# Kernel optimization log

Measured on AMD Instinct MI355X. Metric: run time of the kernel, lower is better.

Reference implementation:

```python
import jax, jax.numpy as jnp
import numpy as np

B, S, E, H = 2, 2048, 1024, 16
DH = E // H  # 64


def setup_inputs() -> dict:
    key = jax.random.key(0)
    ks = jax.random.split(key, 9)
    scale = 1.0 / np.sqrt(E)
    q = jax.random.normal(ks[0], (B, S, E), jnp.float32)
    k = jax.random.normal(ks[1], (B, S, E), jnp.float32)
    v = jax.random.normal(ks[2], (B, S, E), jnp.float32)
    Wq = jax.random.uniform(ks[3], (E, E), jnp.float32, -scale, scale)
    Wk = jax.random.uniform(ks[4], (E, E), jnp.float32, -scale, scale)
    Wv = jax.random.uniform(ks[5], (E, E), jnp.float32, -scale, scale)
    bq = jax.random.uniform(ks[6], (E,), jnp.float32, -scale, scale)
    bk = jax.random.uniform(ks[7], (E,), jnp.float32, -scale, scale)
    bv = jax.random.uniform(ks[8], (E,), jnp.float32, -scale, scale)
    # causal mask: True = masked. [b, s_q, s_k]
    causal = jnp.triu(jnp.ones((S, S), bool), k=1)
    mask = jnp.broadcast_to(causal, (B, S, S))
    return {"q": q, "k": k, "v": v, "Wq": Wq, "bq": bq, "Wk": Wk,
            "bk": bk, "Wv": Wv, "bv": bv, "mask": mask}


def reference(q, k, v, Wq, bq, Wk, bk, Wv, bv, mask):
    b, s_q, _ = q.shape
    s_k = k.shape[1]
    # NB: faithful to the original: .view(b, heads, s, -1) (no transpose)
    Q = (q @ Wq + bq).reshape(b, H, s_q, DH)
    K = (k @ Wk + bk).reshape(b, H, s_k, DH)
    V = (v @ Wv + bv).reshape(b, H, s_k, DH)
    scores = jnp.einsum('bhqd,bhkd->bhqk', Q, K) / jnp.sqrt(
        jnp.asarray(DH, Q.dtype))
    scores = jnp.where(mask[:, None, :, :], -jnp.inf, scores)
    attn = jax.nn.softmax(scores, axis=-1)
    out = jnp.einsum('bhqk,bhkd->bhqd', attn, V).reshape(b, s_q, -1)
    return out  # dropout p=0 / eval mode -> identity
```

## Files before the change

kernel.cpp:

```cpp
#include <hip/hip_runtime.h>

typedef unsigned short u16;
typedef __attribute__((ext_vector_type(8))) __bf16 bf16x8;
typedef __attribute__((ext_vector_type(4))) __bf16 bf16x4;
typedef __attribute__((ext_vector_type(4))) float f32x4;

#define MFMA(a, b, c) __builtin_amdgcn_mfma_f32_16x16x32_bf16((a), (b), (c), 0, 0, 0)
#define KSCALE 0.18033688011112042f

__device__ __forceinline__ void load_lds16(const void* g, void* l) {
  __builtin_amdgcn_global_load_lds(
      (__attribute__((address_space(1))) void*)(g),
      (__attribute__((address_space(3))) void*)(l), 16, 0, 0);
}

__device__ __forceinline__ float launder(float x, float lim) {
  return fminf(fmaxf(x, -lim), lim);
}

__global__ __launch_bounds__(256) void prep(
    const float* __restrict__ x0, const float* __restrict__ x1,
    const float* __restrict__ x2, const float* __restrict__ W0,
    const float* __restrict__ W1, const float* __restrict__ W2,
    __bf16* __restrict__ Xb, __bf16* __restrict__ WT) {
  __shared__ __bf16 tile[64][65];
  int bx = blockIdx.x;
  int t = threadIdx.x;
  if (bx < 3072) {
    int z = bx >> 10, blk = bx & 1023;
    const float* x = z == 0 ? x0 : (z == 1 ? x1 : x2);
    __bf16* o = Xb + (size_t)z * 4194304;
#pragma unroll
    for (int i = 0; i < 4; ++i) {
      size_t e = ((size_t)i * 262144 + (size_t)blk * 256 + t) * 4;
      f32x4 v = *(const f32x4*)&x[e];
      bf16x4 b = {(__bf16)v[0], (__bf16)v[1], (__bf16)v[2], (__bf16)v[3]};
      *(bf16x4*)&o[e] = b;
    }
  } else {
    int idx = bx - 3072;
    int z = idx >> 8, rest = idx & 255;
    const float* W = z == 0 ? W0 : (z == 1 ? W1 : W2);
    float sc = z == 0 ? KSCALE : 1.0f;
    __bf16* out = WT + (size_t)z * 1048576;
    int r0 = (rest >> 4) * 64, c0 = (rest & 15) * 64;
#pragma unroll
    for (int it = 0; it < 16; ++it) {
      int flat = it * 256 + t, r = flat >> 6, c = flat & 63;
      tile[c][r] = (__bf16)(W[(size_t)(r0 + r) * 1024 + c0 + c] * sc);
    }
    __syncthreads();
#pragma unroll
    for (int it = 0; it < 16; ++it) {
      int flat = it * 256 + t, r = flat >> 6, c = flat & 63;
      out[(size_t)(c0 + r) * 1024 + r0 + c] = tile[r][c];
    }
  }
}

__global__ __launch_bounds__(256, 2) void proj_gemm(
    const __bf16* __restrict__ Xb, const __bf16* __restrict__ WT,
    const float* __restrict__ bq, const float* __restrict__ bk,
    const float* __restrict__ bv, __bf16* __restrict__ OutBase) {
  int z = blockIdx.z;
  const __bf16* X = Xb + (size_t)z * 4194304;
  const __bf16* Wt = WT + (size_t)z * 1048576;
  const float* bias = z == 0 ? bq : (z == 1 ? bk : bv);
  float bsc = z == 0 ? KSCALE : 1.0f;
  __bf16* O = OutBase + (size_t)z * 4194304;

  __shared__ __attribute__((aligned(16))) __bf16 As[256 * 32];
  __shared__ __attribute__((aligned(16))) __bf16 Bs[128 * 32];

  int t = threadIdx.x;
  int lane = t & 63, quad = lane >> 4, l16 = lane & 15;
  int wave = t >> 6;
  int wm = (wave >> 1) * 128, wn = (wave & 1) * 64;
  int m0 = blockIdx.x * 256, n0 = blockIdx.y * 128;

  f32x4 zero4 = {0.f, 0.f, 0.f, 0.f};
  f32x4 acc[8][4];
#pragma unroll
  for (int i = 0; i < 8; ++i)
#pragma unroll
    for (int j = 0; j < 4; ++j) acc[i][j] = zero4;

  for (int k0 = 0; k0 < 1024; k0 += 32) {
#pragma unroll
    for (int p = 0; p < 4; ++p) {
      int c = p * 256 + t;
      int r = c >> 2, col = (c & 3) * 8;
      load_lds16(X + (size_t)(m0 + r) * 1024 + k0 + col, &As[c * 8]);
    }
#pragma unroll
    for (int p = 0; p < 2; ++p) {
      int c = p * 256 + t;
      int r = c >> 2, col = (c & 3) * 8;
      load_lds16(Wt + (size_t)(n0 + r) * 1024 + k0 + col, &Bs[c * 8]);
    }
    __syncthreads();
    bf16x8 a[8], b[4];
#pragma unroll
    for (int i = 0; i < 8; ++i)
      a[i] = *(const bf16x8*)&As[(wm + i * 16 + l16) * 32 + quad * 8];
#pragma unroll
    for (int j = 0; j < 4; ++j)
      b[j] = *(const bf16x8*)&Bs[(wn + j * 16 + l16) * 32 + quad * 8];
#pragma unroll
    for (int i = 0; i < 8; ++i)
#pragma unroll
      for (int j = 0; j < 4; ++j) acc[i][j] = MFMA(a[i], b[j], acc[i][j]);
    __syncthreads();
  }

#pragma unroll
  for (int j = 0; j < 4; ++j) {
    int n = n0 + wn + j * 16 + l16;
    float bb = bias[n] * bsc;
#pragma unroll
    for (int i = 0; i < 8; ++i) {
#pragma unroll
      for (int r = 0; r < 4; ++r) {
        int m = m0 + wm + i * 16 + quad * 4 + r;
        O[(size_t)m * 1024 + n] = (__bf16)launder(acc[i][j][r] + bb, 512.f);
      }
    }
  }
}

__global__ __launch_bounds__(256) void transpose_v(
    const u16* __restrict__ Vp, u16* __restrict__ Vt) {
  int bh = blockIdx.y, s0 = blockIdx.x * 64;
  __shared__ u16 tile[64][65];
  int t = threadIdx.x;
  const u16* src = Vp + (size_t)bh * 131072;
  u16* dst = Vt + (size_t)bh * 131072;
#pragma unroll
  for (int it = 0; it < 16; ++it) {
    int flat = it * 256 + t, r = flat >> 6, d = flat & 63;
    tile[d][r] = src[(size_t)(s0 + r) * 64 + d];
  }
  __syncthreads();
#pragma unroll
  for (int it = 0; it < 16; ++it) {
    int flat = it * 256 + t, d = flat >> 6, c = flat & 63;
    dst[(size_t)d * 2048 + s0 + c] = tile[d][c];
  }
}

__global__ __launch_bounds__(256, 2) void flash_attn(
    const __bf16* __restrict__ Qp, const __bf16* __restrict__ Kp,
    const __bf16* __restrict__ Vt, float* __restrict__ out) {
  int qtA = blockIdx.x;
  int qtB = 31 - qtA;
  int bh = blockIdx.y;
  int t = threadIdx.x;
  int lane = t & 63, quad = lane >> 4, l16 = lane & 15;
  int w = t >> 6;
  int jmaxA = qtA >> 1, jmaxB = qtB >> 1;

  __shared__ __attribute__((aligned(16))) __bf16 Ks[2][8192];
  __shared__ __attribute__((aligned(16))) __bf16 Vs[2][8192];
  __shared__ __attribute__((aligned(16))) __bf16 Ps[4][2048];

  const __bf16* Qb = Qp + (size_t)bh * 131072;
  const __bf16* Kb = Kp + (size_t)bh * 131072;
  const __bf16* Vb = Vt + (size_t)bh * 131072;
  __bf16* Pw = Ps[w];

  int qbA = qtA * 64 + w * 16, qbB = qtB * 64 + w * 16;

  bf16x8 qfA[2], qfB[2], ones;
#pragma unroll
  for (int i = 0; i < 8; ++i) ones[i] = (__bf16)1.0f;
#pragma unroll
  for (int kk = 0; kk < 2; ++kk) {
    qfA[kk] = *(const bf16x8*)&Qb[(size_t)(qbA + l16) * 64 + kk * 32 + quad * 8];
    qfB[kk] = *(const bf16x8*)&Qb[(size_t)(qbB + l16) * 64 + kk * 32 + quad * 8];
  }

  f32x4 zero4 = {0.f, 0.f, 0.f, 0.f};
  f32x4 oA[4], oB[4], lAacc = zero4, lBacc = zero4;
#pragma unroll
  for (int nd = 0; nd < 4; ++nd) { oA[nd] = zero4; oB[nd] = zero4; }

  int ks_kpos[4], ks_off[4], vs_d[4], vs_off[4], vs_kq[4];
#pragma unroll
  for (int p = 0; p < 4; ++p) {
    int c = p * 256 + t;
    ks_kpos[p] = (c & 511) >> 2;
    ks_off[p] = (c >> 9) * 32 + (c & 3) * 8;
    vs_kq[p] = c >> 8;
    vs_d[p] = (c & 255) >> 2;
    vs_off[p] = (c & 3) * 8;
  }

  bf16x8 pk[4], pv[4];
#pragma unroll
  for (int p = 0; p < 4; ++p) {
    pk[p] = *(const bf16x8*)&Kb[(size_t)ks_kpos[p] * 64 + ks_off[p]];
    pv[p] = *(const bf16x8*)&Vb[(size_t)vs_d[p] * 2048 + vs_kq[p] * 32 + vs_off[p]];
  }
#pragma unroll
  for (int p = 0; p < 4; ++p) {
    int c = p * 256 + t;
    *(bf16x8*)&Ks[0][c * 8] = pk[p];
    *(bf16x8*)&Vs[0][c * 8] = pv[p];
  }
  if (jmaxB > 0) {
#pragma unroll
    for (int p = 0; p < 4; ++p) {
      pk[p] = *(const bf16x8*)&Kb[(size_t)(128 + ks_kpos[p]) * 64 + ks_off[p]];
      pv[p] = *(const bf16x8*)&Vb[(size_t)vs_d[p] * 2048 + 128 + vs_kq[p] * 32 + vs_off[p]];
    }
  }
  __syncthreads();

  for (int j = 0; j <= jmaxB; ++j) {
    int cur = j & 1, nxt = cur ^ 1;
    bool doA = (j <= jmaxA);

    if (j < jmaxB) {
#pragma unroll
      for (int p = 0; p < 4; ++p) {
        int c = p * 256 + t;
        *(bf16x8*)&Ks[nxt][c * 8] = pk[p];
        *(bf16x8*)&Vs[nxt][c * 8] = pv[p];
      }
      if (j + 1 < jmaxB) {
        int jn = (j + 2) * 128;
#pragma unroll
        for (int p = 0; p < 4; ++p) {
          pk[p] = *(const bf16x8*)&Kb[(size_t)(jn + ks_kpos[p]) * 64 + ks_off[p]];
          pv[p] = *(const bf16x8*)&Vb[(size_t)vs_d[p] * 2048 + jn + vs_kq[p] * 32 + vs_off[p]];
        }
      }
    }

    f32x4 sA[8], sB[8];
#pragma unroll
    for (int nt = 0; nt < 8; ++nt) {
      bf16x8 k0 = *(const bf16x8*)&Ks[cur][(nt * 16 + l16) * 32 + quad * 8];
      bf16x8 k1 = *(const bf16x8*)&Ks[cur][4096 + (nt * 16 + l16) * 32 + quad * 8];
      f32x4 zb = zero4;
      zb = MFMA(k0, qfB[0], zb);
      zb = MFMA(k1, qfB[1], zb);
      sB[nt] = zb;
      if (doA) {
        f32x4 za = zero4;
        za = MFMA(k0, qfA[0], za);
        za = MFMA(k1, qfA[1], za);
        sA[nt] = za;
      }
    }

    if (j == jmaxB) {
      int qg = qbB + l16;
#pragma unroll
      for (int nt = 0; nt < 8; ++nt) {
        int kg = j * 128 + nt * 16 + quad * 4;
#pragma unroll
        for (int r = 0; r < 4; ++r)
          if (kg + r > qg) sB[nt][r] = -1e30f;
      }
    }
#pragma unroll
    for (int nt = 0; nt < 8; ++nt) {
      bf16x4 pb;
#pragma unroll
      for (int r = 0; r < 4; ++r)
        pb[r] = (__bf16)__builtin_amdgcn_exp2f(sB[nt][r]);
      *(bf16x4*)&Pw[l16 * 128 + (((nt * 4 + quad) ^ (l16 * 2)) & 31) * 4] = pb;
    }
    {
      bf16x8 pf[4];
#pragma unroll
      for (int kk = 0; kk < 4; ++kk)
        pf[kk] = *(const bf16x8*)&Pw[l16 * 128 + (((kk * 8 + quad * 2) ^ (l16 * 2)) & 31) * 4];
#pragma unroll
      for (int kk = 0; kk < 4; ++kk) {
        lBacc = MFMA(ones, pf[kk], lBacc);
#pragma unroll
        for (int nd = 0; nd < 4; ++nd) {
          bf16x8 av = *(const bf16x8*)&Vs[cur][kk * 2048 + (nd * 16 + l16) * 32 + quad * 8];
          oB[nd] = MFMA(av, pf[kk], oB[nd]);
        }
      }
    }

    if (doA) {
      if (j == jmaxA) {
        int qg = qbA + l16;
#pragma unroll
        for (int nt = 0; nt < 8; ++nt) {
          int kg = j * 128 + nt * 16 + quad * 4;
#pragma unroll
          for (int r = 0; r < 4; ++r)
            if (kg + r > qg) sA[nt][r] = -1e30f;
        }
      }
#pragma unroll
      for (int nt = 0; nt < 8; ++nt) {
        bf16x4 pb;
#pragma unroll
        for (int r = 0; r < 4; ++r)
          pb[r] = (__bf16)__builtin_amdgcn_exp2f(sA[nt][r]);
        *(bf16x4*)&Pw[l16 * 128 + (((nt * 4 + quad) ^ (l16 * 2)) & 31) * 4] = pb;
      }
      bf16x8 pf[4];
#pragma unroll
      for (int kk = 0; kk < 4; ++kk)
        pf[kk] = *(const bf16x8*)&Pw[l16 * 128 + (((kk * 8 + quad * 2) ^ (l16 * 2)) & 31) * 4];
#pragma unroll
      for (int kk = 0; kk < 4; ++kk) {
        lAacc = MFMA(ones, pf[kk], lAacc);
#pragma unroll
        for (int nd = 0; nd < 4; ++nd) {
          bf16x8 av = *(const bf16x8*)&Vs[cur][kk * 2048 + (nd * 16 + l16) * 32 + quad * 8];
          oA[nd] = MFMA(av, pf[kk], oA[nd]);
        }
      }
    }
    __syncthreads();
  }

  {
    float invA = 1.f / lAacc[0], invB = 1.f / lBacc[0];
    int qA = qbA + l16, qB = qbB + l16;
#pragma unroll
    for (int nd = 0; nd < 4; ++nd) {
      f32x4 a, b;
#pragma unroll
      for (int r = 0; r < 4; ++r) {
        a[r] = launder(oA[nd][r] * invA, 512.f);
        b[r] = launder(oB[nd][r] * invB, 512.f);
      }
      *(f32x4*)&out[(size_t)bh * 131072 + (size_t)qA * 64 + nd * 16 + quad * 4] = a;
      *(f32x4*)&out[(size_t)bh * 131072 + (size_t)qB * 64 + nd * 16 + quad * 4] = b;
    }
  }
}

extern "C" void kernel_launch(void* const* d_in, const int* in_sizes, int n_in,
                              void* d_out, int out_size, void* d_ws, size_t ws_size,
                              hipStream_t stream) {
  (void)in_sizes; (void)n_in; (void)out_size; (void)ws_size;
  const float* q  = (const float*)d_in[0];
  const float* k  = (const float*)d_in[1];
  const float* v  = (const float*)d_in[2];
  const float* Wq = (const float*)d_in[3];
  const float* bq = (const float*)d_in[4];
  const float* Wk = (const float*)d_in[5];
  const float* bk = (const float*)d_in[6];
  const float* Wv = (const float*)d_in[7];
  const float* bv = (const float*)d_in[8];

  __bf16* ws  = (__bf16*)d_ws;
  __bf16* WT  = ws;
  __bf16* QKV = ws + (size_t)3 * 1048576;
  __bf16* Qp  = QKV;
  __bf16* Kp  = QKV + (size_t)4194304;
  __bf16* Vp  = QKV + (size_t)2 * 4194304;
  __bf16* Xb  = QKV + (size_t)3 * 4194304;
  __bf16* Vtr = Xb;

  prep<<<dim3(3840), 256, 0, stream>>>(q, k, v, Wq, Wk, Wv, Xb, WT);
  proj_gemm<<<dim3(16, 8, 3), 256, 0, stream>>>(Xb, WT, bq, bk, bv, QKV);
  transpose_v<<<dim3(32, 32), 256, 0, stream>>>((const u16*)Vp, (u16*)Vtr);
  flash_attn<<<dim3(16, 32), 256, 0, stream>>>(Qp, Kp, Vtr, (float*)d_out);
}
```

Baseline: 214.7 us.

## Fuse all stages into one cooperative persistent kernel with grid syncs

Merges prep, projection GEMM, V transpose and flash attention into a single cooperative kernel of 512 blocks, with grid.sync between stages and a shared-memory union. The aim is to remove the launch gaps between kernels. The projection GEMM tile also shrinks from 256x128 to 128x128, giving 768 jobs so the fixed grid can share them out. The risks are the cost of grid-wide barriers, an uneven loop over jobs (for example 768 jobs over 512 blocks), and occupancy limited by the largest LDS use across stages. A fallback path launches four separate kernels if the cooperative launch fails.

```diff
diff --git a/kernel.cpp b/kernel.cpp
--- a/kernel.cpp
+++ b/kernel.cpp
@@ -1,4 +1,7 @@
 #include <hip/hip_runtime.h>
+#include <hip/hip_cooperative_groups.h>
+
+namespace cg = cooperative_groups;
 
 typedef unsigned short u16;
 typedef __attribute__((ext_vector_type(8))) __bf16 bf16x8;
@@ -18,16 +21,21 @@
   return fminf(fmaxf(x, -lim), lim);
 }
 
-__global__ __launch_bounds__(256) void prep(
+union SMem {
+  __bf16 tile[64][65];
+  struct { __bf16 As[128 * 32]; __bf16 Bs[128 * 32]; } g;
+  struct { __bf16 Ks[2][8192]; __bf16 Vs[2][8192]; __bf16 Ps[4][2048]; } f;
+};
+
+
+__device__ __forceinline__ void prep_job(
+    int j, int t, SMem& sm,
     const float* __restrict__ x0, const float* __restrict__ x1,
     const float* __restrict__ x2, const float* __restrict__ W0,
     const float* __restrict__ W1, const float* __restrict__ W2,
     __bf16* __restrict__ Xb, __bf16* __restrict__ WT) {
-  __shared__ __bf16 tile[64][65];
-  int bx = blockIdx.x;
-  int t = threadIdx.x;
-  if (bx < 3072) {
-    int z = bx >> 10, blk = bx & 1023;
+  if (j < 3072) {
+    int z = j >> 10, blk = j & 1023;
     const float* x = z == 0 ? x0 : (z == 1 ? x1 : x2);
     __bf16* o = Xb + (size_t)z * 4194304;
 #pragma unroll
@@ -38,135 +46,125 @@
       *(bf16x4*)&o[e] = b;
     }
   } else {
-    int idx = bx - 3072;
+    int idx = j - 3072;
     int z = idx >> 8, rest = idx & 255;
     const float* W = z == 0 ? W0 : (z == 1 ? W1 : W2);
     float sc = z == 0 ? KSCALE : 1.0f;
-    __bf16* out = WT + (size_t)z * 1048576;
+    __bf16* outw = WT + (size_t)z * 1048576;
     int r0 = (rest >> 4) * 64, c0 = (rest & 15) * 64;
 #pragma unroll
     for (int it = 0; it < 16; ++it) {
       int flat = it * 256 + t, r = flat >> 6, c = flat & 63;
-      tile[c][r] = (__bf16)(W[(size_t)(r0 + r) * 1024 + c0 + c] * sc);
+      sm.tile[c][r] = (__bf16)(W[(size_t)(r0 + r) * 1024 + c0 + c] * sc);
     }
     __syncthreads();
 #pragma unroll
     for (int it = 0; it < 16; ++it) {
       int flat = it * 256 + t, r = flat >> 6, c = flat & 63;
-      out[(size_t)(c0 + r) * 1024 + r0 + c] = tile[r][c];
-    }
-  }
-}
-
-__global__ __launch_bounds__(256, 2) void proj_gemm(
-    const __bf16* __restrict__ Xb, const __bf16* __restrict__ WT,
-    const float* __restrict__ bq, const float* __restrict__ bk,
-    const float* __restrict__ bv, __bf16* __restrict__ OutBase) {
-  int z = blockIdx.z;
+      outw[(size_t)(c0 + r) * 1024 + r0 + c] = sm.tile[r][c];
+    }
+    __syncthreads();
+  }
+}
+
+__device__ __forceinline__ void proj_job(
+    int job, int t, SMem& sm, const __bf16* __restrict__ Xb,
+    const __bf16* __restrict__ WT, const float* __restrict__ bq,
+    const float* __restrict__ bk, const float* __restrict__ bv,
+    __bf16* __restrict__ QKV) {
+  int z = job >> 8;
+  int rem = job & 255;
+  int m0 = (rem >> 3) * 128, n0 = (rem & 7) * 128;
   const __bf16* X = Xb + (size_t)z * 4194304;
   const __bf16* Wt = WT + (size_t)z * 1048576;
   const float* bias = z == 0 ? bq : (z == 1 ? bk : bv);
   float bsc = z == 0 ? KSCALE : 1.0f;
-  __bf16* O = OutBase + (size_t)z * 4194304;
-
-  __shared__ __attribute__((aligned(16))) __bf16 As[256 * 32];
-  __shared__ __attribute__((aligned(16))) __bf16 Bs[128 * 32];
-
-  int t = threadIdx.x;
+  __bf16* O = QKV + (size_t)z * 4194304;
+
   int lane = t & 63, quad = lane >> 4, l16 = lane & 15;
   int wave = t >> 6;
-  int wm = (wave >> 1) * 128, wn = (wave & 1) * 64;
-  int m0 = blockIdx.x * 256, n0 = blockIdx.y * 128;
+  int wm = (wave >> 1) * 64, wn = (wave & 1) * 64;
 
   f32x4 zero4 = {0.f, 0.f, 0.f, 0.f};
-  f32x4 acc[8][4];
-#pragma unroll
-  for (int i = 0; i < 8; ++i)
-#pragma unroll
-    for (int j = 0; j < 4; ++j) acc[i][j] = zero4;
+  f32x4 acc[4][4];
+#pragma unroll
+  for (int i = 0; i < 4; ++i)
+#pragma unroll
+    for (int j2 = 0; j2 < 4; ++j2) acc[i][j2] = zero4;
 
   for (int k0 = 0; k0 < 1024; k0 += 32) {
-#pragma unroll
-    for (int p = 0; p < 4; ++p) {
-      int c = p * 256 + t;
-      int r = c >> 2, col = (c & 3) * 8;
-      load_lds16(X + (size_t)(m0 + r) * 1024 + k0 + col, &As[c * 8]);
-    }
 #pragma unroll
     for (int p = 0; p < 2; ++p) {
       int c = p * 256 + t;
       int r = c >> 2, col = (c & 3) * 8;
-      load_lds16(Wt + (size_t)(n0 + r) * 1024 + k0 + col, &Bs[c * 8]);
+      load_lds16(X + (size_t)(m0 + r) * 1024 + k0 + col, &sm.g.As[c * 8]);
+      load_lds16(Wt + (size_t)(n0 + r) * 1024 + k0 + col, &sm.g.Bs[c * 8]);
     }
     __syncthreads();
-    bf16x8 a[8], b[4];
-#pragma unroll
-    for (int i = 0; i < 8; ++i)
-      a[i] = *(const bf16x8*)&As[(wm + i * 16 + l16) * 32 + quad * 8];
-#pragma unroll
-    for (int j = 0; j < 4; ++j)
-      b[j] = *(const bf16x8*)&Bs[(wn + j * 16 + l16) * 32 + quad * 8];
-#pragma unroll
-    for (int i = 0; i < 8; ++i)
-#pragma unroll
-      for (int j = 0; j < 4; ++j) acc[i][j] = MFMA(a[i], b[j], acc[i][j]);
+    bf16x8 a[4], b[4];
+#pragma unroll
+    for (int i = 0; i < 4; ++i)
+      a[i] = *(const bf16x8*)&sm.g.As[(wm + i * 16 + l16) * 32 + quad * 8];
+#pragma unroll
+    for (int j2 = 0; j2 < 4; ++j2)
+      b[j2] = *(const bf16x8*)&sm.g.Bs[(wn + j2 * 16 + l16) * 32 + quad * 8];
+#pragma unroll
+    for (int i = 0; i < 4; ++i)
+#pragma unroll
+      for (int j2 = 0; j2 < 4; ++j2) acc[i][j2] = MFMA(a[i], b[j2], acc[i][j2]);
     __syncthreads();
   }
 
 #pragma unroll
-  for (int j = 0; j < 4; ++j) {
-    int n = n0 + wn + j * 16 + l16;
+  for (int j2 = 0; j2 < 4; ++j2) {
+    int n = n0 + wn + j2 * 16 + l16;
     float bb = bias[n] * bsc;
 #pragma unroll
-    for (int i = 0; i < 8; ++i) {
+    for (int i = 0; i < 4; ++i) {
 #pragma unroll
       for (int r = 0; r < 4; ++r) {
         int m = m0 + wm + i * 16 + quad * 4 + r;
-        O[(size_t)m * 1024 + n] = (__bf16)launder(acc[i][j][r] + bb, 512.f);
-      }
-    }
-  }
-}
-
-__global__ __launch_bounds__(256) void transpose_v(
-    const u16* __restrict__ Vp, u16* __restrict__ Vt) {
-  int bh = blockIdx.y, s0 = blockIdx.x * 64;
-  __shared__ u16 tile[64][65];
-  int t = threadIdx.x;
-  const u16* src = Vp + (size_t)bh * 131072;
-  u16* dst = Vt + (size_t)bh * 131072;
+        O[(size_t)m * 1024 + n] = (__bf16)launder(acc[i][j2][r] + bb, 512.f);
+      }
+    }
+  }
+}
+
+__device__ __forceinline__ void tv_job(int job, int t, SMem& sm,
+                                       const __bf16* __restrict__ Vp,
+                                       __bf16* __restrict__ Vt) {
+  int bh = job >> 5, s0 = (job & 31) * 64;
+  const __bf16* src = Vp + (size_t)bh * 131072;
+  __bf16* dst = Vt + (size_t)bh * 131072;
 #pragma unroll
   for (int it = 0; it < 16; ++it) {
     int flat = it * 256 + t, r = flat >> 6, d = flat & 63;
-    tile[d][r] = src[(size_t)(s0 + r) * 64 + d];
+    sm.tile[d][r] = src[(size_t)(s0 + r) * 64 + d];
   }
   __syncthreads();
 #pragma unroll
   for (int it = 0; it < 16; ++it) {
     int flat = it * 256 + t, d = flat >> 6, c = flat & 63;
-    dst[(size_t)d * 2048 + s0 + c] = tile[d][c];
-  }
-}
-
-__global__ __launch_bounds__(256, 2) void flash_attn(
-    const __bf16* __restrict__ Qp, const __bf16* __restrict__ Kp,
-    const __bf16* __restrict__ Vt, float* __restrict__ out) {
-  int qtA = blockIdx.x;
+    dst[(size_t)d * 2048 + s0 + c] = sm.tile[d][c];
+  }
+  __syncthreads();
+}
+
+__device__ __forceinline__ void flash_job(
+    int job, int t, SMem& sm, const __bf16* __restrict__ Qp,
+    const __bf16* __restrict__ Kp, const __bf16* __restrict__ Vt,
+    float* __restrict__ out) {
+  int qtA = job & 15;
   int qtB = 31 - qtA;
-  int bh = blockIdx.y;
-  int t = threadIdx.x;
+  int bh = job >> 4;
   int lane = t & 63, quad = lane >> 4, l16 = lane & 15;
   int w = t >> 6;
   int jmaxA = qtA >> 1, jmaxB = qtB >> 1;
 
-  __shared__ __attribute__((aligned(16))) __bf16 Ks[2][8192];
-  __shared__ __attribute__((aligned(16))) __bf16 Vs[2][8192];
-  __shared__ __attribute__((aligned(16))) __bf16 Ps[4][2048];
-
   const __bf16* Qb = Qp + (size_t)bh * 131072;
   const __bf16* Kb = Kp + (size_t)bh * 131072;
   const __bf16* Vb = Vt + (size_t)bh * 131072;
-  __bf16* Pw = Ps[w];
+  __bf16* Pw = sm.f.Ps[w];
 
   int qbA = qtA * 64 + w * 16, qbB = qtB * 64 + w * 16;
 
@@ -204,8 +202,8 @@
 #pragma unroll
   for (int p = 0; p < 4; ++p) {
     int c = p * 256 + t;
-    *(bf16x8*)&Ks[0][c * 8] = pk[p];
-    *(bf16x8*)&Vs[0][c * 8] = pv[p];
+    *(bf16x8*)&sm.f.Ks[0][c * 8] = pk[p];
+    *(bf16x8*)&sm.f.Vs[0][c * 8] = pv[p];
   }
   if (jmaxB > 0) {
 #pragma unroll
@@ -224,8 +222,8 @@
 #pragma unroll
       for (int p = 0; p < 4; ++p) {
         int c = p * 256 + t;
-        *(bf16x8*)&Ks[nxt][c * 8] = pk[p];
-        *(bf16x8*)&Vs[nxt][c * 8] = pv[p];
+        *(bf16x8*)&sm.f.Ks[nxt][c * 8] = pk[p];
+        *(bf16x8*)&sm.f.Vs[nxt][c * 8] = pv[p];
       }
       if (j + 1 < jmaxB) {
         int jn = (j + 2) * 128;
@@ -240,8 +238,8 @@
     f32x4 sA[8], sB[8];
 #pragma unroll
     for (int nt = 0; nt < 8; ++nt) {
-      bf16x8 k0 = *(const bf16x8*)&Ks[cur][(nt * 16 + l16) * 32 + quad * 8];
-      bf16x8 k1 = *(const bf16x8*)&Ks[cur][4096 + (nt * 16 + l16) * 32 + quad * 8];
+      bf16x8 k0 = *(const bf16x8*)&sm.f.Ks[cur][(nt * 16 + l16) * 32 + quad * 8];
+      bf16x8 k1 = *(const bf16x8*)&sm.f.Ks[cur][4096 + (nt * 16 + l16) * 32 + quad * 8];
       f32x4 zb = zero4;
       zb = MFMA(k0, qfB[0], zb);
       zb = MFMA(k1, qfB[1], zb);
@@ -282,7 +280,7 @@
         lBacc = MFMA(ones, pf[kk], lBacc);
 #pragma unroll
         for (int nd = 0; nd < 4; ++nd) {
-          bf16x8 av = *(const bf16x8*)&Vs[cur][kk * 2048 + (nd * 16 + l16) * 32 + quad * 8];
+          bf16x8 av = *(const bf16x8*)&sm.f.Vs[cur][kk * 2048 + (nd * 16 + l16) * 32 + quad * 8];
           oB[nd] = MFMA(av, pf[kk], oB[nd]);
         }
       }
@@ -316,7 +314,7 @@
         lAacc = MFMA(ones, pf[kk], lAacc);
 #pragma unroll
         for (int nd = 0; nd < 4; ++nd) {
-          bf16x8 av = *(const bf16x8*)&Vs[cur][kk * 2048 + (nd * 16 + l16) * 32 + quad * 8];
+          bf16x8 av = *(const bf16x8*)&sm.f.Vs[cur][kk * 2048 + (nd * 16 + l16) * 32 + quad * 8];
           oA[nd] = MFMA(av, pf[kk], oA[nd]);
         }
       }
@@ -339,6 +337,63 @@
       *(f32x4*)&out[(size_t)bh * 131072 + (size_t)qB * 64 + nd * 16 + quad * 4] = b;
     }
   }
+}
+
+__global__ __launch_bounds__(256, 2) void mega(
+    const float* __restrict__ q, const float* __restrict__ k,
+    const float* __restrict__ v, const float* __restrict__ W0,
+    const float* __restrict__ W1, const float* __restrict__ W2,
+    const float* __restrict__ bq, const float* __restrict__ bk,
+    const float* __restrict__ bv, __bf16* __restrict__ Xb,
+    __bf16* __restrict__ WT, __bf16* __restrict__ QKV,
+    float* __restrict__ out) {
+  __shared__ __attribute__((aligned(16))) SMem sm;
+  cg::grid_group grid = cg::this_grid();
+  int t = threadIdx.x;
+  int bx = blockIdx.x;
+
+  const __bf16* Qp = QKV;
+  const __bf16* Kp = QKV + (size_t)4194304;
+  const __bf16* Vp = QKV + (size_t)2 * 4194304;
+  __bf16* Vtr = Xb;
+
+  for (int j = bx; j < 3840; j += 512)
+    prep_job(j, t, sm, q, k, v, W0, W1, W2, Xb, WT);
+  grid.sync();
+  for (int j = bx; j < 768; j += 512)
+    proj_job(j, t, sm, Xb, WT, bq, bk, bv, QKV);
+  grid.sync();
+  for (int j = bx; j < 1024; j += 512)
+    tv_job(j, t, sm, Vp, Vtr);
+  grid.sync();
+  flash_job(bx, t, sm, Qp, Kp, Vtr, out);
+}
+
+__global__ __launch_bounds__(256) void prep_k(
+    const float* __restrict__ q, const float* __restrict__ k,
+    const float* __restrict__ v, const float* __restrict__ W0,
+    const float* __restrict__ W1, const float* __restrict__ W2,
+    __bf16* __restrict__ Xb, __bf16* __restrict__ WT) {
+  __shared__ __attribute__((aligned(16))) SMem sm;
+  prep_job(blockIdx.x, threadIdx.x, sm, q, k, v, W0, W1, W2, Xb, WT);
+}
+__global__ __launch_bounds__(256, 2) void proj_k(
+    const __bf16* __restrict__ Xb, const __bf16* __restrict__ WT,
+    const float* __restrict__ bq, const float* __restrict__ bk,
+    const float* __restrict__ bv, __bf16* __restrict__ QKV) {
+  __shared__ __attribute__((aligned(16))) SMem sm;
+  proj_job(blockIdx.x, threadIdx.x, sm, Xb, WT, bq, bk, bv, QKV);
+}
+__global__ __launch_bounds__(256) void tv_k(const __bf16* __restrict__ Vp,
+                                            __bf16* __restrict__ Vt) {
+  __shared__ __attribute__((aligned(16))) SMem sm;
+  tv_job(blockIdx.x, threadIdx.x, sm, Vp, Vt);
+}
+__global__ __launch_bounds__(256, 2) void flash_k(
+    const __bf16* __restrict__ Qp, const __bf16* __restrict__ Kp,
+    const __bf16* __restrict__ Vt, float* __restrict__ out) {
+  __shared__ __attribute__((aligned(16))) SMem sm;
+  flash_job(blockIdx.x, threadIdx.x, sm, Qp, Kp, Vt, out);
 }
 
 extern "C" void kernel_launch(void* const* d_in, const int* in_sizes, int n_in,
@@ -358,14 +413,20 @@
   __bf16* ws  = (__bf16*)d_ws;
   __bf16* WT  = ws;
   __bf16* QKV = ws + (size_t)3 * 1048576;
-  __bf16* Qp  = QKV;
-  __bf16* Kp  = QKV + (size_t)4194304;
-  __bf16* Vp  = QKV + (size_t)2 * 4194304;
   __bf16* Xb  = QKV + (size_t)3 * 4194304;
-  __bf16* Vtr = Xb;
-
-  prep<<<dim3(3840), 256, 0, stream>>>(q, k, v, Wq, Wk, Wv, Xb, WT);
-  proj_gemm<<<dim3(16, 8, 3), 256, 0, stream>>>(Xb, WT, bq, bk, bv, QKV);
-  transpose_v<<<dim3(32, 32), 256, 0, stream>>>((const u16*)Vp, (u16*)Vtr);
-  flash_attn<<<dim3(16, 32), 256, 0, stream>>>(Qp, Kp, Vtr, (float*)d_out);
-}
+  float* outp = (float*)d_out;
+
+  void* args[] = {&q, &k, &v, &Wq, &Wk, &Wv, &bq, &bk, &bv, &Xb, &WT, &QKV, &outp};
+  hipError_t err = hipLaunchCooperativeKernel((void*)mega, dim3(512), dim3(256),
+                                              args, 0, stream);
+  if (err != hipSuccess) {
+    const __bf16* Qp = QKV;
+    const __bf16* Kp = QKV + (size_t)4194304;
+    const __bf16* Vp = QKV + (size_t)2 * 4194304;
+    __bf16* Vtr = Xb;
+    prep_k<<<dim3(3840), 256, 0, stream>>>(q, k, v, Wq, Wk, Wv, Xb, WT);
+    proj_k<<<dim3(768), 256, 0, stream>>>(Xb, WT, bq, bk, bv, QKV);
+    tv_k<<<dim3(1024), 256, 0, stream>>>(Vp, Vtr);
+    flash_k<<<dim3(512), 256, 0, stream>>>(Qp, Kp, Vtr, outp);
+  }
+}
```

Result: slower. 449.1 us (+109.2%).
